# Kernel tuning notes

Measured on AMD Instinct MI355X. Metric: run time of the kernel, lower is better.

Reference implementation:

```python
import jax, jax.numpy as jnp
import numpy as np

D_MODEL = 1024
N_HEADS = 16
HEAD_DIM = D_MODEL // N_HEADS  # 64
BUCKET = 64


def setup_inputs() -> dict:
    key = jax.random.key(0)
    k1, k2, k3 = jax.random.split(key, 3)
    B, T = 4, 4096
    x = jax.random.normal(k1, (B, T, D_MODEL), dtype=jnp.float32)
    # torch nn.Linear(d, 3d, bias=False): weight shape (3d, d), y = x @ W.T
    W_qkv = jax.random.normal(k2, (3 * D_MODEL, D_MODEL), dtype=jnp.float32) * (D_MODEL ** -0.5)
    W_out = jax.random.normal(k3, (D_MODEL, D_MODEL), dtype=jnp.float32) * (D_MODEL ** -0.5)
    return {"x": x, "W_qkv": W_qkv, "W_out": W_out}


def reference(x, W_qkv, W_out):
    B, T, _ = x.shape
    qkv = x @ W_qkv.T                                  # [B, T, 3*d_model]
    # split_heads with Hs=head_dim -> [B, 3*nH, T, Hs]; chunk along head axis
    qkv = qkv.reshape(B, T, 3 * N_HEADS, HEAD_DIM).transpose(0, 2, 1, 3)
    q, k, v = jnp.split(qkv, 3, axis=1)                # each [B, nH, T, Hs]

    q = jax.nn.softmax(q, axis=-1) * (HEAD_DIM ** -0.5)
    k = jnp.exp(k)                                     # causal path (mask is None)

    n = T // BUCKET
    bucket = lambda t: t.reshape(B, N_HEADS, n, BUCKET, HEAD_DIM)
    b_q, b_k, b_v = bucket(q), bucket(k), bucket(v)    # [B, H, n, s, d]

    # per-bucket key sums, inclusive cumsum over buckets, then shift to exclusive
    b_k_sum = jnp.sum(b_k, axis=-2)                    # [B, H, n, d]
    b_k_cumsum = jnp.cumsum(b_k_sum, axis=-2)
    b_k_cumsum = jnp.pad(b_k_cumsum, ((0, 0), (0, 0), (1, 0), (0, 0)))[:, :, :-1]

    # per-bucket kv outer products, exclusive cumsum over buckets
    context = jnp.einsum('bhnsd,bhnse->bhnde', b_k, b_v)        # [B, H, n, d, e]
    context = jnp.cumsum(context, axis=-3)
    context = jnp.pad(context, ((0, 0), (0, 0), (1, 0), (0, 0), (0, 0)))[:, :, :-1]

    den = jnp.einsum('bhnsd,bhnd->bhns', b_q, b_k_cumsum)
    D_inv = 1.0 / jnp.maximum(den, 1e-6)
    attn = jnp.einsum('bhnsd,bhnde,bhns->bhnse', b_q, context, D_inv)

    xo = attn.reshape(B, N_HEADS, T, HEAD_DIM)         # [B, H, T, Hs]
    xo = xo.transpose(0, 2, 1, 3).reshape(B, T, D_MODEL)  # cat_heads
    return xo @ W_out.T
```

## Files before the change

### kernel.cpp

```cpp
#include <hip/hip_runtime.h>
#include <hip/hip_bf16.h>
#include <math.h>

typedef __hip_bfloat16 bf16;
typedef __attribute__((ext_vector_type(4))) float f32x4;
typedef __attribute__((ext_vector_type(8))) short bf16x8s;

#define T_SEQ 4096
#define MFMA16(a, b, c) __builtin_amdgcn_mfma_f32_16x16x32_bf16(a, b, c, 0, 0, 0)

static __device__ __forceinline__ float bf2f(short u) {
    return __uint_as_float(((unsigned int)(unsigned short)u) << 16);
}
static __device__ __forceinline__ short f2bf(float f) {
    bf16 h = __float2bfloat16(f);
    union { bf16 b; short s; } c; c.b = h; return c.s;
}
static __device__ __forceinline__ int swz_f(int r) { return (r & 7) ^ (r >> 3); }

__global__ void cvt_f32_bf16(const float* __restrict__ src, bf16* __restrict__ dst, int n8) {
    int i = blockIdx.x * 256 + threadIdx.x;
    if (i >= n8) return;
    f32x4 a = ((const f32x4*)src)[(size_t)i * 2];
    f32x4 b = ((const f32x4*)src)[(size_t)i * 2 + 1];
    union { bf16 h[8]; uint4 u; } p;
    p.h[0] = __float2bfloat16(a.x); p.h[1] = __float2bfloat16(a.y);
    p.h[2] = __float2bfloat16(a.z); p.h[3] = __float2bfloat16(a.w);
    p.h[4] = __float2bfloat16(b.x); p.h[5] = __float2bfloat16(b.y);
    p.h[6] = __float2bfloat16(b.z); p.h[7] = __float2bfloat16(b.w);
    ((uint4*)dst)[i] = p.u;
}

template<int MODE>
__global__ __launch_bounds__(512, 2)
void gemm256(const bf16* __restrict__ A, const bf16* __restrict__ Bm,
             int K, int N,
             bf16* __restrict__ out0, bf16* __restrict__ out1, bf16* __restrict__ out2,
             float* __restrict__ outf)
{
    __shared__ __align__(16) short As[2][2][256 * 32];
    __shared__ __align__(16) short Bs[2][2][256 * 32];
    const int tid  = threadIdx.x;
    const int l    = tid & 63;
    const int wid  = tid >> 6;
    const int wr   = wid >> 2;
    const int wc   = wid & 3;
    const int brow = blockIdx.y * 256;
    const int bcol = blockIdx.x * 256;
    const int nkt  = K >> 6;

    const bf16* Ab = A  + (size_t)brow * K;
    const bf16* Bb = Bm + (size_t)bcol * K;
    const int srow   = tid >> 2;
    const int schunk = tid & 3;

#define STAGE(dstArr, srcp, buf, kh, kt)                                          \
    {                                                                             \
        _Pragma("unroll")                                                         \
        for (int j = 0; j < 2; ++j) {                                             \
            int row = j * 128 + srow;                                             \
            int cs  = schunk ^ ((row >> 1) & 3);                                  \
            const bf16* g = srcp + (size_t)row * K + (kt) * 64 + (kh) * 32 + cs * 8; \
            __builtin_amdgcn_global_load_lds(                                     \
                (const __attribute__((address_space(1))) void*)g,                 \
                (__attribute__((address_space(3))) void*)&dstArr[buf][kh][(j * 512 + tid) * 8], \
                16, 0, 0);                                                        \
        }                                                                         \
    }

    f32x4 acc[8][4];
#pragma unroll
    for (int m = 0; m < 8; ++m)
#pragma unroll
        for (int n = 0; n < 4; ++n) acc[m][n] = (f32x4){0.f, 0.f, 0.f, 0.f};

    STAGE(As, Ab, 0, 0, 0);
    STAGE(Bs, Bb, 0, 0, 0);
    STAGE(As, Ab, 0, 1, 0);
    STAGE(Bs, Bb, 0, 1, 0);
    asm volatile("s_waitcnt vmcnt(4)" ::: "memory");
    __builtin_amdgcn_s_barrier();

    for (int t = 0; t < nkt; ++t) {
        const int cur = t & 1, nxt = cur ^ 1;
        const bool pf = (t + 1 < nkt);
        bf16x8s bfr[4], afr[4];

#define RDA(buf, s, m_) (*(const bf16x8s*)&As[buf][s][(wr * 128 + (m_) * 16 + (l & 15)) * 32 + (((l >> 4) ^ (((wr * 128 + (m_) * 16 + (l & 15)) >> 1) & 3)) * 8)])
#define RDB(buf, s, n_) (*(const bf16x8s*)&Bs[buf][s][(wc * 64 + (n_) * 16 + (l & 15)) * 32 + (((l >> 4) ^ (((wc * 64 + (n_) * 16 + (l & 15)) >> 1) & 3)) * 8)])

#pragma unroll
        for (int n = 0; n < 4; ++n) bfr[n] = RDB(cur, 0, n);
#pragma unroll
        for (int m = 0; m < 4; ++m) afr[m] = RDA(cur, 0, m);
        if (pf) STAGE(As, Ab, nxt, 0, t + 1);
        __builtin_amdgcn_s_barrier();
        asm volatile("s_waitcnt lgkmcnt(0)" ::: "memory");
        __builtin_amdgcn_sched_barrier(0);
        __builtin_amdgcn_s_setprio(1);
#pragma unroll
        for (int m = 0; m < 4; ++m)
#pragma unroll
            for (int n = 0; n < 4; ++n) acc[m][n] = MFMA16(afr[m], bfr[n], acc[m][n]);
        __builtin_amdgcn_s_setprio(0);
        __builtin_amdgcn_s_barrier();

#pragma unroll
        for (int m = 0; m < 4; ++m) afr[m] = RDA(cur, 0, m + 4);
        if (pf) STAGE(Bs, Bb, nxt, 0, t + 1);
        asm volatile("s_waitcnt vmcnt(4)" ::: "memory");
        __builtin_amdgcn_s_barrier();
        asm volatile("s_waitcnt lgkmcnt(0)" ::: "memory");
        __builtin_amdgcn_sched_barrier(0);
        __builtin_amdgcn_s_setprio(1);
#pragma unroll
        for (int m = 0; m < 4; ++m)
#pragma unroll
            for (int n = 0; n < 4; ++n) acc[m + 4][n] = MFMA16(afr[m], bfr[n], acc[m + 4][n]);
        __builtin_amdgcn_s_setprio(0);
        __builtin_amdgcn_s_barrier();

#pragma unroll
        for (int n = 0; n < 4; ++n) bfr[n] = RDB(cur, 1, n);
#pragma unroll
        for (int m = 0; m < 4; ++m) afr[m] = RDA(cur, 1, m);
        if (pf) STAGE(As, Ab, nxt, 1, t + 1);
        __builtin_amdgcn_s_barrier();
        asm volatile("s_waitcnt lgkmcnt(0)" ::: "memory");
        __builtin_amdgcn_sched_barrier(0);
        __builtin_amdgcn_s_setprio(1);
#pragma unroll
        for (int m = 0; m < 4; ++m)
#pragma unroll
            for (int n = 0; n < 4; ++n) acc[m][n] = MFMA16(afr[m], bfr[n], acc[m][n]);
        __builtin_amdgcn_s_setprio(0);
        __builtin_amdgcn_s_barrier();

#pragma unroll
        for (int m = 0; m < 4; ++m) afr[m] = RDA(cur, 1, m + 4);
        if (pf) STAGE(Bs, Bb, nxt, 1, t + 1);
        asm volatile("s_waitcnt vmcnt(4)" ::: "memory");
        __builtin_amdgcn_s_barrier();
        asm volatile("s_waitcnt lgkmcnt(0)" ::: "memory");
        __builtin_amdgcn_sched_barrier(0);
        __builtin_amdgcn_s_setprio(1);
#pragma unroll
        for (int m = 0; m < 4; ++m)
#pragma unroll
            for (int n = 0; n < 4; ++n) acc[m + 4][n] = MFMA16(afr[m], bfr[n], acc[m + 4][n]);
        __builtin_amdgcn_s_setprio(0);
        __builtin_amdgcn_s_barrier();
    }

    const int region = bcol >> 10;
#pragma unroll
    for (int m = 0; m < 8; ++m) {
        int row = brow + wr * 128 + m * 16 + ((l >> 4) << 2);
#pragma unroll
        for (int n = 0; n < 4; ++n) {
            int col = bcol + wc * 64 + n * 16 + (l & 15);
#pragma unroll
            for (int r = 0; r < 4; ++r) {
                float v = acc[m][n][r];
                size_t rr = (size_t)(row + r);
                if (MODE == 1) {
                    outf[rr * N + col] = v;
                } else {
                    int c = col & 1023;
                    if (region == 0)      out0[rr * 1024 + c] = __float2bfloat16(v);
                    else if (region == 1) out1[rr * 1024 + c] = __float2bfloat16(__expf(v));
                    else                  out2[rr * 1024 + c] = __float2bfloat16(v);
                }
            }
        }
    }
#undef STAGE
#undef RDA
#undef RDB
}

__global__ __launch_bounds__(256)
void bucket_kv(const bf16* __restrict__ Kb, const bf16* __restrict__ Vb,
               bf16* __restrict__ ctxb, float* __restrict__ ksum)
{
    __shared__ __align__(16) short k_t[64 * 64];
    __shared__ __align__(16) short v_t[64 * 64];
    __shared__ __align__(16) float ct[64 * 68];
    const int bid = blockIdx.x;
    const int bh = bid >> 6, n = bid & 63;
    const int b = bh >> 4, h = bh & 15;
    const size_t rowbase = (size_t)(b * T_SEQ + n * 64) * 1024 + h * 64;
    const int tid = threadIdx.x;

#pragma unroll
    for (int half = 0; half < 2; ++half) {
        int s  = (tid >> 3) + half * 32;
        int dc = tid & 7;
        bf16x8s kv = *(const bf16x8s*)&Kb[rowbase + (size_t)s * 1024 + dc * 8];
        bf16x8s vv = *(const bf16x8s*)&Vb[rowbase + (size_t)s * 1024 + dc * 8];
        int sc = s >> 3, slo = s & 7;
#pragma unroll
        for (int u = 0; u < 8; ++u) {
            int d = dc * 8 + u;
            int addr = d * 64 + (((sc) ^ swz_f(d)) << 3) + slo;
            k_t[addr] = ((short*)&kv)[u];
            v_t[addr] = ((short*)&vv)[u];
        }
    }
    __syncthreads();

    const int l = tid & 63, w = tid >> 6;

    if (tid < 64) {
        int d = tid;
        float s = 0.f;
#pragma unroll
        for (int c = 0; c < 8; ++c) {
            bf16x8s kk = *(const bf16x8s*)&k_t[d * 64 + ((c ^ swz_f(d)) << 3)];
#pragma unroll
            for (int u = 0; u < 8; ++u) s += bf2f(((short*)&kk)[u]);
        }
        ksum[(size_t)bid * 64 + d] = s;
    }

    f32x4 acc[4];
#pragma unroll
    for (int i = 0; i < 4; ++i) acc[i] = (f32x4){0.f, 0.f, 0.f, 0.f};
    bf16x8s afr[2], bfr[2][4];
#pragma unroll
    for (int kk = 0; kk < 2; ++kk) {
        int cc = kk * 4 + (l >> 4);
        int r = w * 16 + (l & 15);
        afr[kk] = *(const bf16x8s*)&k_t[r * 64 + ((cc ^ swz_f(r)) << 3)];
#pragma unroll
        for (int n4 = 0; n4 < 4; ++n4) {
            int e = n4 * 16 + (l & 15);
            bfr[kk][n4] = *(const bf16x8s*)&v_t[e * 64 + ((cc ^ swz_f(e)) << 3)];
        }
    }
#pragma unroll
    for (int kk = 0; kk < 2; ++kk)
#pragma unroll
        for (int n4 = 0; n4 < 4; ++n4)
            acc[n4] = MFMA16(afr[kk], bfr[kk][n4], acc[n4]);

#pragma unroll
    for (int n4 = 0; n4 < 4; ++n4) {
        int e = n4 * 16 + (l & 15);
        int d0 = w * 16 + ((l >> 4) << 2);
        *(f32x4*)&ct[e * 68 + d0] = acc[n4];
    }
    __syncthreads();

#pragma unroll
    for (int j = 0; j < 2; ++j) {
        int i = tid + 256 * j;
        int e = i >> 3, d0 = (i & 7) * 8;
        f32x4 lo = *(const f32x4*)&ct[e * 68 + d0];
        f32x4 hi = *(const f32x4*)&ct[e * 68 + d0 + 4];
        union { short h[8]; uint4 u; } p;
        p.h[0] = f2bf(lo.x); p.h[1] = f2bf(lo.y); p.h[2] = f2bf(lo.z); p.h[3] = f2bf(lo.w);
        p.h[4] = f2bf(hi.x); p.h[5] = f2bf(hi.y); p.h[6] = f2bf(hi.z); p.h[7] = f2bf(hi.w);
        ((uint4*)&ctxb[(size_t)bid * 4096])[i] = p.u;
    }
}

__global__ void cumsum_excl(const bf16* __restrict__ ctxb, const float* __restrict__ ksum,
                            bf16* __restrict__ ctp, float* __restrict__ ksump)
{
    const int bh = blockIdx.y;
    if (blockIdx.x == 4) {
        int d = threadIdx.x;
        if (d >= 64) return;
        float run = 0.f;
        for (int j = 0; j < 64; ++j) {
            size_t idx = (size_t)(bh * 64 + j) * 64 + d;
            float v = ksum[idx];
            ksump[idx] = run;
            run += v;
        }
        return;
    }
    int e0 = (blockIdx.x * 256 + threadIdx.x) * 4;
    float r0 = 0.f, r1 = 0.f, r2 = 0.f, r3 = 0.f;
    for (int j = 0; j < 64; ++j) {
        size_t idx = (size_t)(bh * 64 + j) * 4096 + e0;
        ushort4 v = *(const ushort4*)&ctxb[idx];
        ushort4 o;
        o.x = (ushort)f2bf(r0); o.y = (ushort)f2bf(r1);
        o.z = (ushort)f2bf(r2); o.w = (ushort)f2bf(r3);
        *(ushort4*)&ctp[idx] = o;
        r0 += bf2f((short)v.x); r1 += bf2f((short)v.y);
        r2 += bf2f((short)v.z); r3 += bf2f((short)v.w);
    }
}

__global__ __launch_bounds__(256)
void bucket_attn(const bf16* __restrict__ Qb, const bf16* __restrict__ ctp,
                 const float* __restrict__ ksump, bf16* __restrict__ attn)
{
    __shared__ __align__(16) short q_bf[64 * 64];
    __shared__ __align__(16) short ct_bf[64 * 64];
    __shared__ __align__(16) short at_s[64 * 72];
    __shared__ float dinv_s[64];
    __shared__ float ksum_s[64];
    const int bid = blockIdx.x;
    const int bh = bid >> 6, n = bid & 63;
    const int b = bh >> 4, h = bh & 15;
    const size_t rowbase = (size_t)(b * T_SEQ + n * 64) * 1024 + h * 64;
    const int tid = threadIdx.x;
    const int l = tid & 63, w = tid >> 6;

#pragma unroll
    for (int j = 0; j < 2; ++j) {
        int i = tid + 256 * j;
        int e = i >> 3, dc = i & 7;
        bf16x8s cv = *(const bf16x8s*)&ctp[(size_t)bid * 4096 + e * 64 + dc * 8];
        *(bf16x8s*)&ct_bf[e * 64 + ((dc ^ swz_f(e)) << 3)] = cv;
    }
    if (tid < 64) ksum_s[tid] = ksump[(size_t)bid * 64 + tid];
    __syncthreads();

#pragma unroll
    for (int i = 0; i < 16; ++i) {
        int s = w * 16 + i;
        float x = bf2f(*(const short*)&Qb[rowbase + (size_t)s * 1024 + l]);
        float mx = x;
#pragma unroll
        for (int off = 32; off; off >>= 1) mx = fmaxf(mx, __shfl_xor(mx, off));
        float ex = __expf(x - mx);
        float sm = ex;
#pragma unroll
        for (int off = 32; off; off >>= 1) sm += __shfl_xor(sm, off);
        float qv = ex / sm * 0.125f;
        float dp = qv * ksum_s[l];
#pragma unroll
        for (int off = 32; off; off >>= 1) dp += __shfl_xor(dp, off);
        if (l == 0) dinv_s[s] = 1.f / fmaxf(dp, 1e-6f);
        q_bf[s * 64 + ((((l >> 3)) ^ swz_f(s)) << 3) + (l & 7)] = f2bf(qv);
    }
    __syncthreads();

    f32x4 acc[4];
#pragma unroll
    for (int i = 0; i < 4; ++i) acc[i] = (f32x4){0.f, 0.f, 0.f, 0.f};
    bf16x8s afr[2], bfr[2][4];
#pragma unroll
    for (int kk = 0; kk < 2; ++kk) {
        int cc = kk * 4 + (l >> 4);
        int r = w * 16 + (l & 15);
        afr[kk] = *(const bf16x8s*)&q_bf[r * 64 + ((cc ^ swz_f(r)) << 3)];
#pragma unroll
        for (int n4 = 0; n4 < 4; ++n4) {
            int e = n4 * 16 + (l & 15);
            bfr[kk][n4] = *(const bf16x8s*)&ct_bf[e * 64 + ((cc ^ swz_f(e)) << 3)];
        }
    }
#pragma unroll
    for (int kk = 0; kk < 2; ++kk)
#pragma unroll
        for (int n4 = 0; n4 < 4; ++n4)
            acc[n4] = MFMA16(afr[kk], bfr[kk][n4], acc[n4]);

#pragma unroll
    for (int n4 = 0; n4 < 4; ++n4) {
        int e = n4 * 16 + (l & 15);
#pragma unroll
        for (int r = 0; r < 4; ++r) {
            int s = w * 16 + ((l >> 4) << 2) + r;
            at_s[s * 72 + e] = f2bf(acc[n4][r] * dinv_s[s]);
        }
    }
    __syncthreads();

#pragma unroll
    for (int j = 0; j < 2; ++j) {
        int i = tid + 256 * j;
        int s = i >> 3, c = i & 7;
        bf16x8s v = *(const bf16x8s*)&at_s[s * 72 + c * 8];
        *(bf16x8s*)&attn[rowbase + (size_t)s * 1024 + c * 8] = v;
    }
}

extern "C" void kernel_launch(void* const* d_in, const int* in_sizes, int n_in,
                              void* d_out, int out_size, void* d_ws, size_t ws_size,
                              hipStream_t stream)
{
    const float* x    = (const float*)d_in[0];
    const float* Wqkv = (const float*)d_in[1];
    const float* Wout = (const float*)d_in[2];

    char* ws = (char*)d_ws;
    size_t off = 0;
    auto alloc = [&](size_t bytes) { void* p = ws + off; off += (bytes + 255) & ~(size_t)255; return p; };
    bf16*  xb    = (bf16*)alloc((size_t)16384 * 1024 * 2);
    bf16*  wqkvb = (bf16*)alloc((size_t)3072 * 1024 * 2);
    bf16*  woutb = (bf16*)alloc((size_t)1024 * 1024 * 2);
    bf16*  Qb    = (bf16*)alloc((size_t)16384 * 1024 * 2);
    bf16*  Kb    = (bf16*)alloc((size_t)16384 * 1024 * 2);
    bf16*  Vb    = (bf16*)alloc((size_t)16384 * 1024 * 2);
    bf16*  ctxb  = (bf16*)alloc((size_t)4096 * 4096 * 2);
    float* ksum  = (float*)alloc((size_t)4096 * 64 * 4);
    bf16*  ctp   = (bf16*)alloc((size_t)4096 * 4096 * 2);
    float* ksump = (float*)alloc((size_t)4096 * 64 * 4);
    bf16*  attnb = xb;
    float* outf  = (float*)d_out;

    cvt_f32_bf16<<<dim3(16384 * 1024 / 8 / 256), 256, 0, stream>>>(x, xb, 16384 * 1024 / 8);
    cvt_f32_bf16<<<dim3(3072 * 1024 / 8 / 256), 256, 0, stream>>>(Wqkv, wqkvb, 3072 * 1024 / 8);
    cvt_f32_bf16<<<dim3(1024 * 1024 / 8 / 256), 256, 0, stream>>>(Wout, woutb, 1024 * 1024 / 8);

    gemm256<0><<<dim3(12, 64), 512, 0, stream>>>(xb, wqkvb, 1024, 3072, Qb, Kb, Vb, nullptr);
    bucket_kv<<<dim3(4096), 256, 0, stream>>>(Kb, Vb, ctxb, ksum);
    cumsum_excl<<<dim3(5, 64), 256, 0, stream>>>(ctxb, ksum, ctp, ksump);
    bucket_attn<<<dim3(4096), 256, 0, stream>>>(Qb, ctp, ksump, attnb);
    gemm256<1><<<dim3(4, 64), 512, 0, stream>>>(attnb, woutb, 1024, 1024, nullptr, nullptr, nullptr, outf);
}
```

Before: 283.8 us.

## Stage QKV GEMM epilogue through LDS for vectorized stores and swizzle block order

Merges the A/B shared buffers into one flat LDS array so the bf16 QKV epilogue can reuse it: each half of the tile's rows is written to LDS, then copied out with 16-byte vector stores instead of scattered 2-byte stores. It also remaps the block index so consecutive workgroups are interleaved in groups of 8, which is meant to improve L2 reuse of A and B tiles. The cost is extra LDS traffic and two barriers per half in the epilogue.

```diff
diff --git a/kernel.cpp b/kernel.cpp
--- a/kernel.cpp
+++ b/kernel.cpp
@@ -38,15 +38,21 @@
              bf16* __restrict__ out0, bf16* __restrict__ out1, bf16* __restrict__ out2,
              float* __restrict__ outf)
 {
-    __shared__ __align__(16) short As[2][2][256 * 32];
-    __shared__ __align__(16) short Bs[2][2][256 * 32];
+    __shared__ __align__(16) short SMEM[65536];
     const int tid  = threadIdx.x;
     const int l    = tid & 63;
     const int wid  = tid >> 6;
     const int wr   = wid >> 2;
     const int wc   = wid & 3;
-    const int brow = blockIdx.y * 256;
-    const int bcol = blockIdx.x * 256;
+
+    const int nwg  = gridDim.x * gridDim.y;
+    const int flat = blockIdx.y * gridDim.x + blockIdx.x;
+    const int swzb = (flat & 7) * (nwg >> 3) + (flat >> 3);
+    const int bx   = swzb % gridDim.x;
+    const int by   = swzb / gridDim.x;
+
+    const int brow = by * 256;
+    const int bcol = bx * 256;
     const int nkt  = K >> 6;
 
     const bf16* Ab = A  + (size_t)brow * K;
@@ -54,7 +60,7 @@
     const int srow   = tid >> 2;
     const int schunk = tid & 3;
 
-#define STAGE(dstArr, srcp, buf, kh, kt)                                          \
+#define STAGE(isB, srcp, buf, kh, kt)                                             \
     {                                                                             \
         _Pragma("unroll")                                                         \
         for (int j = 0; j < 2; ++j) {                                             \
@@ -63,10 +69,12 @@
             const bf16* g = srcp + (size_t)row * K + (kt) * 64 + (kh) * 32 + cs * 8; \
             __builtin_amdgcn_global_load_lds(                                     \
                 (const __attribute__((address_space(1))) void*)g,                 \
-                (__attribute__((address_space(3))) void*)&dstArr[buf][kh][(j * 512 + tid) * 8], \
+                (__attribute__((address_space(3))) void*)&SMEM[(isB) * 32768 + ((buf) * 2 + (kh)) * 8192 + (j * 512 + tid) * 8], \
                 16, 0, 0);                                                        \
         }                                                                         \
     }
+#define RDA(buf, s, m_) (*(const bf16x8s*)&SMEM[((buf) * 2 + (s)) * 8192 + (wr * 128 + (m_) * 16 + (l & 15)) * 32 + (((l >> 4) ^ (((wr * 128 + (m_) * 16 + (l & 15)) >> 1) & 3)) * 8)])
+#define RDB(buf, s, n_) (*(const bf16x8s*)&SMEM[32768 + ((buf) * 2 + (s)) * 8192 + (wc * 64 + (n_) * 16 + (l & 15)) * 32 + (((l >> 4) ^ (((wc * 64 + (n_) * 16 + (l & 15)) >> 1) & 3)) * 8)])
 
     f32x4 acc[8][4];
 #pragma unroll
@@ -74,10 +82,10 @@
 #pragma unroll
         for (int n = 0; n < 4; ++n) acc[m][n] = (f32x4){0.f, 0.f, 0.f, 0.f};
 
-    STAGE(As, Ab, 0, 0, 0);
-    STAGE(Bs, Bb, 0, 0, 0);
-    STAGE(As, Ab, 0, 1, 0);
-    STAGE(Bs, Bb, 0, 1, 0);
+    STAGE(0, Ab, 0, 0, 0);
+    STAGE(1, Bb, 0, 0, 0);
+    STAGE(0, Ab, 0, 1, 0);
+    STAGE(1, Bb, 0, 1, 0);
     asm volatile("s_waitcnt vmcnt(4)" ::: "memory");
     __builtin_amdgcn_s_barrier();
 
@@ -86,14 +94,11 @@
         const bool pf = (t + 1 < nkt);
         bf16x8s bfr[4], afr[4];
 
-#define RDA(buf, s, m_) (*(const bf16x8s*)&As[buf][s][(wr * 128 + (m_) * 16 + (l & 15)) * 32 + (((l >> 4) ^ (((wr * 128 + (m_) * 16 + (l & 15)) >> 1) & 3)) * 8)])
-#define RDB(buf, s, n_) (*(const bf16x8s*)&Bs[buf][s][(wc * 64 + (n_) * 16 + (l & 15)) * 32 + (((l >> 4) ^ (((wc * 64 + (n_) * 16 + (l & 15)) >> 1) & 3)) * 8)])
-
 #pragma unroll
         for (int n = 0; n < 4; ++n) bfr[n] = RDB(cur, 0, n);
 #pragma unroll
         for (int m = 0; m < 4; ++m) afr[m] = RDA(cur, 0, m);
-        if (pf) STAGE(As, Ab, nxt, 0, t + 1);
+        if (pf) STAGE(0, Ab, nxt, 0, t + 1);
         __builtin_amdgcn_s_barrier();
         asm volatile("s_waitcnt lgkmcnt(0)" ::: "memory");
         __builtin_amdgcn_sched_barrier(0);
@@ -107,7 +112,7 @@
 
 #pragma unroll
         for (int m = 0; m < 4; ++m) afr[m] = RDA(cur, 0, m + 4);
-        if (pf) STAGE(Bs, Bb, nxt, 0, t + 1);
+        if (pf) STAGE(1, Bb, nxt, 0, t + 1);
         asm volatile("s_waitcnt vmcnt(4)" ::: "memory");
         __builtin_amdgcn_s_barrier();
         asm volatile("s_waitcnt lgkmcnt(0)" ::: "memory");
@@ -124,7 +129,7 @@
         for (int n = 0; n < 4; ++n) bfr[n] = RDB(cur, 1, n);
 #pragma unroll
         for (int m = 0; m < 4; ++m) afr[m] = RDA(cur, 1, m);
-        if (pf) STAGE(As, Ab, nxt, 1, t + 1);
+        if (pf) STAGE(0, Ab, nxt, 1, t + 1);
         __builtin_amdgcn_s_barrier();
         asm volatile("s_waitcnt lgkmcnt(0)" ::: "memory");
         __builtin_amdgcn_sched_barrier(0);
@@ -138,7 +143,7 @@
 
 #pragma unroll
         for (int m = 0; m < 4; ++m) afr[m] = RDA(cur, 1, m + 4);
-        if (pf) STAGE(Bs, Bb, nxt, 1, t + 1);
+        if (pf) STAGE(1, Bb, nxt, 1, t + 1);
         asm volatile("s_waitcnt vmcnt(4)" ::: "memory");
         __builtin_amdgcn_s_barrier();
         asm volatile("s_waitcnt lgkmcnt(0)" ::: "memory");
@@ -152,26 +157,52 @@
         __builtin_amdgcn_s_barrier();
     }
 
-    const int region = bcol >> 10;
-#pragma unroll
-    for (int m = 0; m < 8; ++m) {
-        int row = brow + wr * 128 + m * 16 + ((l >> 4) << 2);
-#pragma unroll
-        for (int n = 0; n < 4; ++n) {
-            int col = bcol + wc * 64 + n * 16 + (l & 15);
-#pragma unroll
-            for (int r = 0; r < 4; ++r) {
-                float v = acc[m][n][r];
-                size_t rr = (size_t)(row + r);
-                if (MODE == 1) {
-                    outf[rr * N + col] = v;
-                } else {
-                    int c = col & 1023;
-                    if (region == 0)      out0[rr * 1024 + c] = __float2bfloat16(v);
-                    else if (region == 1) out1[rr * 1024 + c] = __float2bfloat16(__expf(v));
-                    else                  out2[rr * 1024 + c] = __float2bfloat16(v);
+    if (MODE == 1) {
+#pragma unroll
+        for (int m = 0; m < 8; ++m) {
+            int row = brow + wr * 128 + m * 16 + ((l >> 4) << 2);
+#pragma unroll
+            for (int n = 0; n < 4; ++n) {
+                int col = bcol + wc * 64 + n * 16 + (l & 15);
+#pragma unroll
+                for (int r = 0; r < 4; ++r)
+                    outf[(size_t)(row + r) * N + col] = acc[m][n][r];
+            }
+        }
+    } else {
+        const int region = bcol >> 10;
+        const int cbase  = bcol & 1023;
+        bf16* dst = (region == 0) ? out0 : (region == 1) ? out1 : out2;
+#pragma unroll
+        for (int h = 0; h < 2; ++h) {
+            if (wr == h) {
+#pragma unroll
+                for (int m = 0; m < 8; ++m) {
+                    int rl = m * 16 + ((l >> 4) << 2);
+#pragma unroll
+                    for (int n = 0; n < 4; ++n) {
+                        int col = wc * 64 + n * 16 + (l & 15);
+#pragma unroll
+                        for (int r = 0; r < 4; ++r) {
+                            float v = acc[m][n][r];
+                            if (region == 1) v = __expf(v);
+                            SMEM[(rl + r) * 264 + col] = f2bf(v);
+                        }
+                    }
                 }
             }
+            __syncthreads();
+            {
+                int row = tid >> 2;
+                int cc  = (tid & 3) * 64;
+                size_t gb = (size_t)(brow + h * 128 + row) * 1024 + cbase + cc;
+#pragma unroll
+                for (int j = 0; j < 8; ++j) {
+                    bf16x8s vv = *(const bf16x8s*)&SMEM[row * 264 + cc + j * 8];
+                    *(bf16x8s*)&dst[gb + j * 8] = vv;
+                }
+            }
+            __syncthreads();
         }
     }
 #undef STAGE
```

Measured after the change: 297.2 us. 4.7% more time.
